# Performance work log

Hardware: AMD Instinct MI355X
Metric: run time of the kernel (lower is better)

## Reference

```python
import jax, jax.numpy as jnp
import numpy as np

N_NODES = 100000
N_EDGES = 1250000
N_FEAT = 128
NHID = 64
NUM_GRAPHS = 256


def setup_inputs() -> dict:
    key = jax.random.key(0)
    ks = jax.random.split(key, 12)
    sc = lambda fan_in: 1.414 * (6.0 / fan_in) ** 0.5  # rough xavier-ish scale
    inp = {
        "x": jax.random.normal(ks[0], (N_NODES, N_FEAT), dtype=jnp.float32),
        "edge_attr": jax.random.uniform(ks[1], (N_EDGES, 5), dtype=jnp.float32),
        "W_e1": jax.random.normal(ks[2], (5, NHID), dtype=jnp.float32) * sc(5),
        "b_e1": jnp.zeros((NHID,), jnp.float32),
        "W_e2": jax.random.normal(ks[3], (NHID, NHID), dtype=jnp.float32) * sc(NHID),
        "b_e2": jnp.zeros((NHID,), jnp.float32),
        "W_e3": jax.random.normal(ks[4], (NHID, 1), dtype=jnp.float32) * sc(NHID),
        "b_e3": jnp.zeros((1,), jnp.float32),
        "W_g": jax.random.normal(ks[5], (N_FEAT, NHID), dtype=jnp.float32) * sc(N_FEAT),
        "b_g": jnp.zeros((NHID,), jnp.float32),
        "W_b1": jax.random.normal(ks[6], (NHID, NHID), dtype=jnp.float32) * sc(NHID),
        "b_b1": jnp.zeros((NHID,), jnp.float32),
        "W_b2": jax.random.normal(ks[7], (NHID, 1), dtype=jnp.float32) * sc(NHID),
        "b_b2": jnp.zeros((1,), jnp.float32),
        "edge_index": jax.random.randint(ks[8], (2, N_EDGES), 0, N_NODES, dtype=jnp.int64 if jax.config.jax_enable_x64 else jnp.int32),
        "batch": jnp.sort(jax.random.randint(ks[9], (N_NODES,), 0, NUM_GRAPHS, dtype=jnp.int64 if jax.config.jax_enable_x64 else jnp.int32)),
    }
    return inp


def _forward(x, edge_attr, W_e1, b_e1, W_e2, b_e2, W_e3, b_e3, W_g, b_g,
             W_b1, b_b1, W_b2, b_b2, edge_index, batch):
    N = x.shape[0]
    # edge MLP -> scalar weight per edge, then final ReLU (F.relu in forward)
    h = jax.nn.relu(edge_attr @ W_e1 + b_e1)
    h = jax.nn.relu(h @ W_e2 + b_e2)
    edge_w = jax.nn.relu((h @ W_e3 + b_e3)[:, 0])  # [E]

    row, col = edge_index[0], edge_index[1]
    # add self-loops with weight 1 (PyG GCNConv default)
    loop = jnp.arange(N, dtype=row.dtype)
    row_f = jnp.concatenate([row, loop])
    col_f = jnp.concatenate([col, loop])
    w_f = jnp.concatenate([edge_w, jnp.ones((N,), edge_w.dtype)])

    # symmetric normalization D^{-1/2} A_hat D^{-1/2}
    deg = jax.ops.segment_sum(w_f, col_f, num_segments=N)
    dinv = jnp.where(deg > 0, jax.lax.rsqrt(jnp.where(deg > 0, deg, 1.0)), 0.0)
    norm = dinv[row_f] * w_f * dinv[col_f]  # [E+N]

    xw = x @ W_g  # [N, nhid]
    agg = jax.ops.segment_sum(xw[row_f] * norm[:, None], col_f, num_segments=N)
    node = jax.nn.relu(agg + b_g)  # dropout is identity in eval mode

    pooled = jax.ops.segment_sum(node, batch, num_segments=NUM_GRAPHS)  # [G, nhid]
    z = jax.nn.relu(pooled @ W_b1 + b_b1)
    logits = z @ W_b2 + b_b2  # [G, 1]
    return logits


def reference(x, edge_attr, W_e1, b_e1, W_e2, b_e2, W_e3, b_e3, W_g, b_g,
              W_b1, b_b1, W_b2, b_b2, edge_index, batch):
    return _forward(x, edge_attr, W_e1, b_e1, W_e2, b_e2, W_e3, b_e3, W_g, b_g,
                    W_b1, b_b1, W_b2, b_b2, edge_index, batch)
```

## Files before the change

### kernel.cpp

```cpp
#include <hip/hip_runtime.h>
#include <hip/hip_bf16.h>

#define N_NODES 100000
#define N_EDGES 1250000
#define N_FEAT 128
#define NHID 64
#define NUM_GRAPHS 256
#define CAP 32

typedef __attribute__((ext_vector_type(8))) short short8;
typedef __attribute__((ext_vector_type(16))) float float16;

static __device__ __forceinline__ short f2bf(float x) {
    __hip_bfloat16 b = __float2bfloat16(x);
    return *reinterpret_cast<short*>(&b);
}
static __device__ __forceinline__ float bf2f(unsigned short s) {
    __hip_bfloat16 b = *reinterpret_cast<__hip_bfloat16*>(&s);
    return __bfloat162float(b);
}
static __device__ __forceinline__ int rho(int s) {
    int r = s & 12;
    if (r == 4) return s + 4;
    if (r == 8) return s - 4;
    return s;
}
static __device__ __forceinline__ int uperm(int m) {
    return (m & ~15) | rho(m & 15);
}

__global__ __launch_bounds__(256) void k1_edge_mlp(
    const float* __restrict__ ea, const float* __restrict__ W1,
    const float* __restrict__ b1, const float* __restrict__ W2,
    const float* __restrict__ b2, const float* __restrict__ W3,
    const float* __restrict__ b3, float* __restrict__ edge_w)
{
    const int lane = threadIdx.x & 63;
    const int l31 = lane & 31;
    const int h = lane >> 5;
    const int wslot = blockIdx.x * 4 + (threadIdx.x >> 6);
    const int S = gridDim.x * 4;
    const float b3v = b3[0];

    short8 a1hi[2], a1lo[2];
    #pragma unroll
    for (int t = 0; t < 2; ++t)
        #pragma unroll
        for (int j = 0; j < 8; ++j) {
            int k = 8 * h + j;
            int m = uperm(t * 32 + l31);
            float v = (k < 5) ? W1[k * NHID + m] : ((k == 5) ? b1[m] : 0.0f);
            short hi = f2bf(v);
            a1hi[t][j] = hi;
            a1lo[t][j] = f2bf(v - bf2f((unsigned short)hi));
        }

    short8 afrag[2][4];
    #pragma unroll
    for (int t = 0; t < 2; ++t)
        #pragma unroll
        for (int kk = 0; kk < 4; ++kk)
            #pragma unroll
            for (int j = 0; j < 8; ++j) {
                int k = kk * 16 + h * 8 + j;
                afrag[t][kk][j] = f2bf(W2[k * NHID + t * 32 + l31]);
            }

    short8 a2b[2], bone;
    #pragma unroll
    for (int t = 0; t < 2; ++t)
        #pragma unroll
        for (int j = 0; j < 8; ++j)
            a2b[t][j] = (h == 0 && j == 0) ? f2bf(b2[t * 32 + l31]) : (short)0;
    #pragma unroll
    for (int j = 0; j < 8; ++j)
        bone[j] = (h == 0 && j == 0) ? f2bf(1.0f) : (short)0;

    float w3r[2][16];
    #pragma unroll
    for (int t = 0; t < 2; ++t)
        #pragma unroll
        for (int r = 0; r < 16; ++r)
            w3r[t][r] = W3[t * 32 + (r & 3) + 8 * (r >> 2) + 4 * h];

    const int NCHUNK = (N_EDGES + 31) / 32;

    for (int chunk = wslot; chunk < NCHUNK; chunk += S) {
        int e = chunk * 32 + l31;
        bool valid = e < N_EDGES;
        int ec = valid ? e : (N_EDGES - 1);

        short8 behi, belo;
        #pragma unroll
        for (int j = 0; j < 8; ++j) {
            float v = 0.0f;
            if (h == 0) {
                if (j < 5) v = ea[ec * 5 + j];
                else if (j == 5) v = 1.0f;
            }
            short hi = f2bf(v);
            behi[j] = hi;
            belo[j] = (h == 0 && j < 5) ? f2bf(v - bf2f((unsigned short)hi)) : (short)0;
        }

        float16 A1[2];
        #pragma unroll
        for (int t = 0; t < 2; ++t)
            #pragma unroll
            for (int r = 0; r < 16; ++r) A1[t][r] = 0.0f;
        #pragma unroll
        for (int t = 0; t < 2; ++t) {
            A1[t] = __builtin_amdgcn_mfma_f32_32x32x16_bf16(a1hi[t], behi, A1[t], 0, 0, 0);
            A1[t] = __builtin_amdgcn_mfma_f32_32x32x16_bf16(a1hi[t], belo, A1[t], 0, 0, 0);
            A1[t] = __builtin_amdgcn_mfma_f32_32x32x16_bf16(a1lo[t], behi, A1[t], 0, 0, 0);
        }

        short8 bf2v[4];
        #pragma unroll
        for (int kk = 0; kk < 4; ++kk) {
            int t = kk >> 1;
            int o = 8 * (kk & 1);
            #pragma unroll
            for (int j = 0; j < 8; ++j)
                bf2v[kk][j] = f2bf(fmaxf(A1[t][o + j], 0.0f));
        }

        float16 C0, C1;
        #pragma unroll
        for (int r = 0; r < 16; ++r) { C0[r] = 0.0f; C1[r] = 0.0f; }
        #pragma unroll
        for (int kk = 0; kk < 4; ++kk) {
            C0 = __builtin_amdgcn_mfma_f32_32x32x16_bf16(afrag[0][kk], bf2v[kk], C0, 0, 0, 0);
            C1 = __builtin_amdgcn_mfma_f32_32x32x16_bf16(afrag[1][kk], bf2v[kk], C1, 0, 0, 0);
        }
        C0 = __builtin_amdgcn_mfma_f32_32x32x16_bf16(a2b[0], bone, C0, 0, 0, 0);
        C1 = __builtin_amdgcn_mfma_f32_32x32x16_bf16(a2b[1], bone, C1, 0, 0, 0);

        float partial = 0.0f;
        #pragma unroll
        for (int r = 0; r < 16; ++r) {
            partial += fmaxf(C0[r], 0.0f) * w3r[0][r];
            partial += fmaxf(C1[r], 0.0f) * w3r[1][r];
        }
        float total = partial + __shfl_xor(partial, 32, 64);
        float w = fmaxf(total + b3v, 0.0f);

        if (h == 0 && valid) edge_w[e] = w;
    }
}

__global__ void kB_place(const float* __restrict__ edge_w,
                         const int* __restrict__ eidx,
                         int* __restrict__ cnt, int2* __restrict__ recs) {
    int e = blockIdx.x * 256 + threadIdx.x;
    if (e >= N_EDGES) return;
    float w = edge_w[e];
    if (w <= 0.0f) return;
    int col = eidx[N_EDGES + e];
    int pos = atomicAdd(&cnt[col], 1);
    if (pos < CAP) recs[(size_t)col * CAP + pos] = make_int2(eidx[e], __float_as_int(w));
}

__global__ void kC_dinv(const int* __restrict__ cnt, const int2* __restrict__ recs,
                        float* __restrict__ dinv) {
    int n = blockIdx.x * 256 + threadIdx.x;
    if (n >= N_NODES) return;
    int m = min(cnt[n], CAP);
    float s = 1.0f;
    for (int j = 0; j < m; ++j) s += __int_as_float(recs[(size_t)n * CAP + j].y);
    dinv[n] = rsqrtf(s);
}

__global__ __launch_bounds__(256) void k3_xw(
    const float* __restrict__ x, const float* __restrict__ Wg,
    unsigned short* __restrict__ xw)
{
    const int lane = threadIdx.x & 63;
    const int l31 = lane & 31;
    const int h = lane >> 5;
    const int wslot = blockIdx.x * 4 + (threadIdx.x >> 6);

    short8 bw[8][2];
    #pragma unroll
    for (int kk = 0; kk < 8; ++kk)
        #pragma unroll
        for (int u = 0; u < 2; ++u)
            #pragma unroll
            for (int j = 0; j < 8; ++j)
                bw[kk][u][j] = f2bf(Wg[(kk * 16 + 8 * h + j) * NHID + u * 32 + l31]);

    const int NC = N_NODES / 32;
    for (int chunk = wslot; chunk < NC; chunk += gridDim.x * 4) {
        int base = chunk * 32;
        const float* xrow = x + (size_t)(base + l31) * N_FEAT + 8 * h;

        float16 acc0, acc1;
        #pragma unroll
        for (int r = 0; r < 16; ++r) { acc0[r] = 0.0f; acc1[r] = 0.0f; }

        #pragma unroll
        for (int kk = 0; kk < 8; ++kk) {
            float4 p = *(const float4*)(xrow + kk * 16);
            float4 q = *(const float4*)(xrow + kk * 16 + 4);
            short8 af;
            af[0] = f2bf(p.x); af[1] = f2bf(p.y); af[2] = f2bf(p.z); af[3] = f2bf(p.w);
            af[4] = f2bf(q.x); af[5] = f2bf(q.y); af[6] = f2bf(q.z); af[7] = f2bf(q.w);
            acc0 = __builtin_amdgcn_mfma_f32_32x32x16_bf16(af, bw[kk][0], acc0, 0, 0, 0);
            acc1 = __builtin_amdgcn_mfma_f32_32x32x16_bf16(af, bw[kk][1], acc1, 0, 0, 0);
        }

        #pragma unroll
        for (int r = 0; r < 16; ++r) {
            int node = base + (r & 3) + 8 * (r >> 2) + 4 * h;
            xw[(size_t)node * NHID + l31] = (unsigned short)f2bf(acc0[r]);
            xw[(size_t)node * NHID + 32 + l31] = (unsigned short)f2bf(acc1[r]);
        }
    }
}

__global__ __launch_bounds__(256) void kD_gather_pool(
    const int* __restrict__ cnt, const int2* __restrict__ recs,
    const unsigned short* __restrict__ xw, const float* __restrict__ dinv,
    const float* __restrict__ bg, const int* __restrict__ batch,
    float* __restrict__ pooled)
{
    const int lane = threadIdx.x & 63;
    const int wv = blockIdx.x * 4 + (threadIdx.x >> 6);
    int n0 = wv * 4;
    if (n0 >= N_NODES) return;
    int n1 = min(n0 + 4, N_NODES);
    float bgl = bg[lane];
    float pacc = 0.0f;
    int curg = batch[n0];
    for (int n = n0; n < n1; ++n) {
        int g = batch[n];
        if (g != curg) {
            atomicAdd(&pooled[curg * NHID + lane], pacc);
            pacc = 0.0f;
            curg = g;
        }
        int m = min(cnt[n], CAP);
        const int2* rb = recs + (size_t)n * CAP;
        float dvn = dinv[n];
        float acc = bf2f(xw[(size_t)n * NHID + lane]) * dvn;
        int j = 0;
        for (; j + 4 <= m; j += 4) {
            int2 r0 = rb[j], r1 = rb[j + 1], r2 = rb[j + 2], r3 = rb[j + 3];
            float w0 = __int_as_float(r0.y) * dinv[r0.x];
            float w1 = __int_as_float(r1.y) * dinv[r1.x];
            float w2 = __int_as_float(r2.y) * dinv[r2.x];
            float w3 = __int_as_float(r3.y) * dinv[r3.x];
            float g0 = bf2f(xw[(size_t)r0.x * NHID + lane]);
            float g1 = bf2f(xw[(size_t)r1.x * NHID + lane]);
            float g2 = bf2f(xw[(size_t)r2.x * NHID + lane]);
            float g3 = bf2f(xw[(size_t)r3.x * NHID + lane]);
            acc = fmaf(w0, g0, acc);
            acc = fmaf(w1, g1, acc);
            acc = fmaf(w2, g2, acc);
            acc = fmaf(w3, g3, acc);
        }
        for (; j < m; ++j) {
            int2 r = rb[j];
            float w = __int_as_float(r.y) * dinv[r.x];
            acc = fmaf(w, bf2f(xw[(size_t)r.x * NHID + lane]), acc);
        }
        pacc += fmaxf(acc * dvn + bgl, 0.0f);
    }
    atomicAdd(&pooled[curg * NHID + lane], pacc);
}

__global__ __launch_bounds__(64) void kE_final(
    const float* __restrict__ pooled, const float* __restrict__ Wb1,
    const float* __restrict__ bb1, const float* __restrict__ Wb2,
    const float* __restrict__ bb2, float* __restrict__ out) {
    __shared__ float p[NHID];
    int lane = threadIdx.x;
    int g = blockIdx.x;
    p[lane] = pooled[g * NHID + lane];
    __syncthreads();
    float z = bb1[lane];
    #pragma unroll
    for (int k = 0; k < NHID; ++k) z += p[k] * Wb1[k * NHID + lane];
    z = fmaxf(z, 0.0f) * Wb2[lane];
    #pragma unroll
    for (int off = 32; off > 0; off >>= 1)
        z += __shfl_down(z, off, 64);
    if (lane == 0) out[g] = z + bb2[0];
}

extern "C" void kernel_launch(void* const* d_in, const int* in_sizes, int n_in,
                              void* d_out, int out_size, void* d_ws, size_t ws_size,
                              hipStream_t stream) {
    const float* x        = (const float*)d_in[0];
    const float* ea       = (const float*)d_in[1];
    const float* W_e1     = (const float*)d_in[2];
    const float* b_e1     = (const float*)d_in[3];
    const float* W_e2     = (const float*)d_in[4];
    const float* b_e2     = (const float*)d_in[5];
    const float* W_e3     = (const float*)d_in[6];
    const float* b_e3     = (const float*)d_in[7];
    const float* W_g      = (const float*)d_in[8];
    const float* b_g      = (const float*)d_in[9];
    const float* W_b1     = (const float*)d_in[10];
    const float* b_b1     = (const float*)d_in[11];
    const float* W_b2     = (const float*)d_in[12];
    const float* b_b2     = (const float*)d_in[13];
    const int*   eidx     = (const int*)d_in[14];
    const int*   batch    = (const int*)d_in[15];
    float* out = (float*)d_out;

    char* wsb = (char*)d_ws;
    int*   cnt    = (int*)wsb;
    float* pooled = (float*)(wsb + 4 * 100000);
    float* edge_w = (float*)(wsb + 4 * 116480);
    float* dinv   = (float*)(wsb + 4 * 1366480);
    int2*  recs   = (int2*)(wsb + 4 * 1466496);
    unsigned short* xw = (unsigned short*)(wsb + 4 * 7866496);

    hipMemsetAsync(wsb, 0, 4 * 116384, stream);

    k1_edge_mlp<<<dim3(2048), dim3(256), 0, stream>>>(
        ea, W_e1, b_e1, W_e2, b_e2, W_e3, b_e3, edge_w);
    kB_place<<<dim3((N_EDGES + 255) / 256), dim3(256), 0, stream>>>(
        edge_w, eidx, cnt, recs);
    kC_dinv<<<dim3((N_NODES + 255) / 256), dim3(256), 0, stream>>>(cnt, recs, dinv);
    k3_xw<<<dim3(782), dim3(256), 0, stream>>>(x, W_g, xw);
    kD_gather_pool<<<dim3(6250), dim3(256), 0, stream>>>(
        cnt, recs, xw, dinv, b_g, batch, pooled);
    kE_final<<<dim3(NUM_GRAPHS), dim3(64), 0, stream>>>(pooled, W_b1, b_b1, W_b2, b_b2, out);
}
```

Measured before the change: 212.4 us.

## Fuse edge MLP, XW projection and workspace zeroing into one kernel

Combines the edge-MLP kernel, the x@W_g MFMA kernel and the workspace memset into a single persistent kernel that dispatches work chunks by index range. This removes two launches and a memset, and lets the compute-bound edge work overlap the bandwidth-bound XW work. In exchange, the W_g fragments are now reloaded and converted to bf16 from global memory for every node chunk instead of once per wave, and register pressure rises from the merged code paths.

```diff
diff --git a/kernel.cpp b/kernel.cpp
--- a/kernel.cpp
+++ b/kernel.cpp
@@ -8,6 +8,12 @@
 #define NUM_GRAPHS 256
 #define CAP 32
 
+#define NE_CH 39063
+#define NN_CH 3125
+#define NZ_CH 29
+#define NTOT (NE_CH + NN_CH + NZ_CH)
+#define ZERO_WORDS 116384
+
 typedef __attribute__((ext_vector_type(8))) short short8;
 typedef __attribute__((ext_vector_type(16))) float float16;
 
@@ -29,11 +35,13 @@
     return (m & ~15) | rho(m & 15);
 }
 
-__global__ __launch_bounds__(256) void k1_edge_mlp(
+__global__ __launch_bounds__(256) void kA(
     const float* __restrict__ ea, const float* __restrict__ W1,
     const float* __restrict__ b1, const float* __restrict__ W2,
     const float* __restrict__ b2, const float* __restrict__ W3,
-    const float* __restrict__ b3, float* __restrict__ edge_w)
+    const float* __restrict__ b3, float* __restrict__ edge_w,
+    const float* __restrict__ x, const float* __restrict__ Wg,
+    unsigned short* __restrict__ xw, int* __restrict__ zbase)
 {
     const int lane = threadIdx.x & 63;
     const int l31 = lane & 31;
@@ -83,69 +91,110 @@
         for (int r = 0; r < 16; ++r)
             w3r[t][r] = W3[t * 32 + (r & 3) + 8 * (r >> 2) + 4 * h];
 
-    const int NCHUNK = (N_EDGES + 31) / 32;
-
-    for (int chunk = wslot; chunk < NCHUNK; chunk += S) {
-        int e = chunk * 32 + l31;
-        bool valid = e < N_EDGES;
-        int ec = valid ? e : (N_EDGES - 1);
-
-        short8 behi, belo;
-        #pragma unroll
-        for (int j = 0; j < 8; ++j) {
-            float v = 0.0f;
-            if (h == 0) {
-                if (j < 5) v = ea[ec * 5 + j];
-                else if (j == 5) v = 1.0f;
-            }
-            short hi = f2bf(v);
-            behi[j] = hi;
-            belo[j] = (h == 0 && j < 5) ? f2bf(v - bf2f((unsigned short)hi)) : (short)0;
-        }
-
-        float16 A1[2];
-        #pragma unroll
-        for (int t = 0; t < 2; ++t)
-            #pragma unroll
-            for (int r = 0; r < 16; ++r) A1[t][r] = 0.0f;
-        #pragma unroll
-        for (int t = 0; t < 2; ++t) {
-            A1[t] = __builtin_amdgcn_mfma_f32_32x32x16_bf16(a1hi[t], behi, A1[t], 0, 0, 0);
-            A1[t] = __builtin_amdgcn_mfma_f32_32x32x16_bf16(a1hi[t], belo, A1[t], 0, 0, 0);
-            A1[t] = __builtin_amdgcn_mfma_f32_32x32x16_bf16(a1lo[t], behi, A1[t], 0, 0, 0);
-        }
-
-        short8 bf2v[4];
-        #pragma unroll
-        for (int kk = 0; kk < 4; ++kk) {
-            int t = kk >> 1;
-            int o = 8 * (kk & 1);
-            #pragma unroll
-            for (int j = 0; j < 8; ++j)
-                bf2v[kk][j] = f2bf(fmaxf(A1[t][o + j], 0.0f));
-        }
-
-        float16 C0, C1;
-        #pragma unroll
-        for (int r = 0; r < 16; ++r) { C0[r] = 0.0f; C1[r] = 0.0f; }
-        #pragma unroll
-        for (int kk = 0; kk < 4; ++kk) {
-            C0 = __builtin_amdgcn_mfma_f32_32x32x16_bf16(afrag[0][kk], bf2v[kk], C0, 0, 0, 0);
-            C1 = __builtin_amdgcn_mfma_f32_32x32x16_bf16(afrag[1][kk], bf2v[kk], C1, 0, 0, 0);
-        }
-        C0 = __builtin_amdgcn_mfma_f32_32x32x16_bf16(a2b[0], bone, C0, 0, 0, 0);
-        C1 = __builtin_amdgcn_mfma_f32_32x32x16_bf16(a2b[1], bone, C1, 0, 0, 0);
-
-        float partial = 0.0f;
-        #pragma unroll
-        for (int r = 0; r < 16; ++r) {
-            partial += fmaxf(C0[r], 0.0f) * w3r[0][r];
-            partial += fmaxf(C1[r], 0.0f) * w3r[1][r];
-        }
-        float total = partial + __shfl_xor(partial, 32, 64);
-        float w = fmaxf(total + b3v, 0.0f);
-
-        if (h == 0 && valid) edge_w[e] = w;
+    for (int chunk = wslot; chunk < NTOT; chunk += S) {
+        if (chunk < NE_CH) {
+            int e = chunk * 32 + l31;
+            bool valid = e < N_EDGES;
+            int ec = valid ? e : (N_EDGES - 1);
+
+            short8 behi, belo;
+            #pragma unroll
+            for (int j = 0; j < 8; ++j) {
+                float v = 0.0f;
+                if (h == 0) {
+                    if (j < 5) v = ea[ec * 5 + j];
+                    else if (j == 5) v = 1.0f;
+                }
+                short hi = f2bf(v);
+                behi[j] = hi;
+                belo[j] = (h == 0 && j < 5) ? f2bf(v - bf2f((unsigned short)hi)) : (short)0;
+            }
+
+            float16 A1[2];
+            #pragma unroll
+            for (int t = 0; t < 2; ++t)
+                #pragma unroll
+                for (int r = 0; r < 16; ++r) A1[t][r] = 0.0f;
+            #pragma unroll
+            for (int t = 0; t < 2; ++t) {
+                A1[t] = __builtin_amdgcn_mfma_f32_32x32x16_bf16(a1hi[t], behi, A1[t], 0, 0, 0);
+                A1[t] = __builtin_amdgcn_mfma_f32_32x32x16_bf16(a1hi[t], belo, A1[t], 0, 0, 0);
+                A1[t] = __builtin_amdgcn_mfma_f32_32x32x16_bf16(a1lo[t], behi, A1[t], 0, 0, 0);
+            }
+
+            short8 bf2v[4];
+            #pragma unroll
+            for (int kk = 0; kk < 4; ++kk) {
+                int t = kk >> 1;
+                int o = 8 * (kk & 1);
+                #pragma unroll
+                for (int j = 0; j < 8; ++j)
+                    bf2v[kk][j] = f2bf(fmaxf(A1[t][o + j], 0.0f));
+            }
+
+            float16 C0, C1;
+            #pragma unroll
+            for (int r = 0; r < 16; ++r) { C0[r] = 0.0f; C1[r] = 0.0f; }
+            #pragma unroll
+            for (int kk = 0; kk < 4; ++kk) {
+                C0 = __builtin_amdgcn_mfma_f32_32x32x16_bf16(afrag[0][kk], bf2v[kk], C0, 0, 0, 0);
+                C1 = __builtin_amdgcn_mfma_f32_32x32x16_bf16(afrag[1][kk], bf2v[kk], C1, 0, 0, 0);
+            }
+            C0 = __builtin_amdgcn_mfma_f32_32x32x16_bf16(a2b[0], bone, C0, 0, 0, 0);
+            C1 = __builtin_amdgcn_mfma_f32_32x32x16_bf16(a2b[1], bone, C1, 0, 0, 0);
+
+            float partial = 0.0f;
+            #pragma unroll
+            for (int r = 0; r < 16; ++r) {
+                partial += fmaxf(C0[r], 0.0f) * w3r[0][r];
+                partial += fmaxf(C1[r], 0.0f) * w3r[1][r];
+            }
+            float total = partial + __shfl_xor(partial, 32, 64);
+            float w = fmaxf(total + b3v, 0.0f);
+
+            if (h == 0 && valid) edge_w[e] = w;
+        } else if (chunk < NE_CH + NN_CH) {
+            int slot = chunk - NE_CH;
+            int base = slot * 32;
+            const float* xrow = x + (size_t)(base + l31) * N_FEAT + 8 * h;
+
+            float16 acc0, acc1;
+            #pragma unroll
+            for (int r = 0; r < 16; ++r) { acc0[r] = 0.0f; acc1[r] = 0.0f; }
+
+            #pragma unroll
+            for (int kk = 0; kk < 8; ++kk) {
+                float4 p = *(const float4*)(xrow + kk * 16);
+                float4 q = *(const float4*)(xrow + kk * 16 + 4);
+                short8 b0, b1f;
+                #pragma unroll
+                for (int j = 0; j < 8; ++j) {
+                    const float* wgp = Wg + (kk * 16 + 8 * h + j) * NHID;
+                    b0[j]  = f2bf(wgp[l31]);
+                    b1f[j] = f2bf(wgp[32 + l31]);
+                }
+                short8 af;
+                af[0] = f2bf(p.x); af[1] = f2bf(p.y); af[2] = f2bf(p.z); af[3] = f2bf(p.w);
+                af[4] = f2bf(q.x); af[5] = f2bf(q.y); af[6] = f2bf(q.z); af[7] = f2bf(q.w);
+                acc0 = __builtin_amdgcn_mfma_f32_32x32x16_bf16(af, b0, acc0, 0, 0, 0);
+                acc1 = __builtin_amdgcn_mfma_f32_32x32x16_bf16(af, b1f, acc1, 0, 0, 0);
+            }
+
+            #pragma unroll
+            for (int r = 0; r < 16; ++r) {
+                int node = base + (r & 3) + 8 * (r >> 2) + 4 * h;
+                xw[(size_t)node * NHID + l31] = (unsigned short)f2bf(acc0[r]);
+                xw[(size_t)node * NHID + 32 + l31] = (unsigned short)f2bf(acc1[r]);
+            }
+        } else {
+            int zc = chunk - NE_CH - NN_CH;
+            int base = zc * 4096;
+            #pragma unroll
+            for (int i = 0; i < 64; ++i) {
+                int idx = base + i * 64 + lane;
+                if (idx < ZERO_WORDS) zbase[idx] = 0;
+            }
+        }
     }
 }
 
@@ -169,53 +218,6 @@
     float s = 1.0f;
     for (int j = 0; j < m; ++j) s += __int_as_float(recs[(size_t)n * CAP + j].y);
     dinv[n] = rsqrtf(s);
-}
-
-__global__ __launch_bounds__(256) void k3_xw(
-    const float* __restrict__ x, const float* __restrict__ Wg,
-    unsigned short* __restrict__ xw)
-{
-    const int lane = threadIdx.x & 63;
-    const int l31 = lane & 31;
-    const int h = lane >> 5;
-    const int wslot = blockIdx.x * 4 + (threadIdx.x >> 6);
-
-    short8 bw[8][2];
-    #pragma unroll
-    for (int kk = 0; kk < 8; ++kk)
-        #pragma unroll
-        for (int u = 0; u < 2; ++u)
-            #pragma unroll
-            for (int j = 0; j < 8; ++j)
-                bw[kk][u][j] = f2bf(Wg[(kk * 16 + 8 * h + j) * NHID + u * 32 + l31]);
-
-    const int NC = N_NODES / 32;
-    for (int chunk = wslot; chunk < NC; chunk += gridDim.x * 4) {
-        int base = chunk * 32;
-        const float* xrow = x + (size_t)(base + l31) * N_FEAT + 8 * h;
-
-        float16 acc0, acc1;
-        #pragma unroll
-        for (int r = 0; r < 16; ++r) { acc0[r] = 0.0f; acc1[r] = 0.0f; }
-
-        #pragma unroll
-        for (int kk = 0; kk < 8; ++kk) {
-            float4 p = *(const float4*)(xrow + kk * 16);
-            float4 q = *(const float4*)(xrow + kk * 16 + 4);
-            short8 af;
-            af[0] = f2bf(p.x); af[1] = f2bf(p.y); af[2] = f2bf(p.z); af[3] = f2bf(p.w);
-            af[4] = f2bf(q.x); af[5] = f2bf(q.y); af[6] = f2bf(q.z); af[7] = f2bf(q.w);
-            acc0 = __builtin_amdgcn_mfma_f32_32x32x16_bf16(af, bw[kk][0], acc0, 0, 0, 0);
-            acc1 = __builtin_amdgcn_mfma_f32_32x32x16_bf16(af, bw[kk][1], acc1, 0, 0, 0);
-        }
-
-        #pragma unroll
-        for (int r = 0; r < 16; ++r) {
-            int node = base + (r & 3) + 8 * (r >> 2) + 4 * h;
-            xw[(size_t)node * NHID + l31] = (unsigned short)f2bf(acc0[r]);
-            xw[(size_t)node * NHID + 32 + l31] = (unsigned short)f2bf(acc1[r]);
-        }
-    }
 }
 
 __global__ __launch_bounds__(256) void kD_gather_pool(
@@ -317,14 +319,11 @@
     int2*  recs   = (int2*)(wsb + 4 * 1466496);
     unsigned short* xw = (unsigned short*)(wsb + 4 * 7866496);
 
-    hipMemsetAsync(wsb, 0, 4 * 116384, stream);
-
-    k1_edge_mlp<<<dim3(2048), dim3(256), 0, stream>>>(
-        ea, W_e1, b_e1, W_e2, b_e2, W_e3, b_e3, edge_w);
+    kA<<<dim3(2048), dim3(256), 0, stream>>>(
+        ea, W_e1, b_e1, W_e2, b_e2, W_e3, b_e3, edge_w, x, W_g, xw, (int*)wsb);
     kB_place<<<dim3((N_EDGES + 255) / 256), dim3(256), 0, stream>>>(
         edge_w, eidx, cnt, recs);
     kC_dinv<<<dim3((N_NODES + 255) / 256), dim3(256), 0, stream>>>(cnt, recs, dinv);
-    k3_xw<<<dim3(782), dim3(256), 0, stream>>>(x, W_g, xw);
     kD_gather_pool<<<dim3(6250), dim3(256), 0, stream>>>(
         cnt, recs, xw, dinv, b_g, batch, pooled);
     kE_final<<<dim3(NUM_GRAPHS), dim3(64), 0, stream>>>(pooled, W_b1, b_b1, W_b2, b_b2, out);
```

New measurement: 251.9 us. +18.6%, slower.
